# Optimization experiments

Hardware: AMD Instinct MI355X
Metric: run time of the kernel (lower is better)

## Reference

```python
import jax, jax.numpy as jnp
import numpy as np

N = 8192
IN_F = 256
OUT_F = 128

def setup_inputs() -> dict:
    key = jax.random.key(0)
    k1, k2, k3, k4, k5 = jax.random.split(key, 5)
    adjacency_matrix = jax.random.uniform(k1, (N, N), dtype=jnp.float32)
    node_features = jax.random.normal(k2, (N, IN_F), dtype=jnp.float32)
    # nn.Linear(in_features, out_features): W is [out, in], b is [out]
    W = jax.random.normal(k3, (OUT_F, IN_F), dtype=jnp.float32) / np.sqrt(IN_F)
    b = jax.random.normal(k4, (OUT_F,), dtype=jnp.float32) * 0.01
    attn_weights = jax.random.normal(k5, (OUT_F, OUT_F), dtype=jnp.float32)
    return {"adjacency_matrix": adjacency_matrix, "node_features": node_features,
            "W": W, "b": b, "attn_weights": attn_weights}

def reference(adjacency_matrix, node_features, W, b, attn_weights):
    # h = Linear(node_features): [N, out]
    h = node_features @ W.T + b
    # bilinear scores: h @ (A @ h^T) -> [N, N]
    scores = jnp.einsum('nd,de,me->nm', h, attn_weights, h)
    attn = jax.nn.softmax(scores, axis=1)
    # weighted aggregation: [N, N] @ [N, out]
    h_agg = attn @ h
    return h_agg
```

## Files before the change

kernel.cpp:

```cpp
#include <hip/hip_runtime.h>
#include <hip/hip_bf16.h>
#include <stdint.h>


#define NN 8192
#define INF_ 256
#define D 128
#define BQ 128
#define BK 64
#define KSPLIT 8
#define KSEG (NN / KSPLIT)
#define NTILE (KSEG / BK)
#define L2E 1.44269504088896340736f

typedef __attribute__((ext_vector_type(8))) short bf16x8;
typedef __attribute__((ext_vector_type(8))) unsigned short u16x8;
typedef __attribute__((ext_vector_type(4))) float f32x4;

__device__ __forceinline__ void gld16(const __hip_bfloat16* g, __hip_bfloat16* l) {
    __builtin_amdgcn_global_load_lds(
        (const __attribute__((address_space(1))) unsigned int*)(unsigned long long)(uintptr_t)g,
        (__attribute__((address_space(3))) unsigned int*)(unsigned long long)(uintptr_t)l,
        16, 0, 0);
}

__device__ __forceinline__ size_t k_img(int grow, int c) {
    const int row = grow & 63;
    return (size_t)(grow >> 6) * 8192 + row * 128 + (((c >> 3) ^ (row & 15)) * 8) + (c & 7);
}

__device__ __forceinline__ size_t v_img(int j, int c) {
    const int jj = j & 63;
    const int jt = (jj >> 4) & 3, q = (jj >> 2) & 3, r = jj & 3;
    const int jp = (jt >> 1) * 32 + q * 8 + (jt & 1) * 4 + r;
    return (size_t)(j >> 6) * 8192 + c * 64 + (((jp >> 3) ^ (c & 7)) * 8) + (jp & 7);
}

__global__ __launch_bounds__(256) void prep_kernel(
    const float* __restrict__ X, const float* __restrict__ W,
    const float* __restrict__ bias, const float* __restrict__ A,
    __hip_bfloat16* __restrict__ h_hi, __hip_bfloat16* __restrict__ h_lo,
    __hip_bfloat16* __restrict__ q_hi, __hip_bfloat16* __restrict__ q_lo,
    __hip_bfloat16* __restrict__ htp)
{
    __shared__ float xs[32][INF_];
    __shared__ float hs[32][D];
    const int tid  = threadIdx.x;
    const int row0 = blockIdx.x * 32;

    {
        const f32x4* Xv = (const f32x4*)(X + (size_t)row0 * INF_);
        f32x4* xsv = (f32x4*)&xs[0][0];
        #pragma unroll
        for (int i = 0; i < 8; ++i) xsv[tid + i*256] = Xv[tid + i*256];
    }
    __syncthreads();

    const int c  = tid & 127;
    const int rh = tid >> 7;

    float acc[16];
    #pragma unroll
    for (int r = 0; r < 16; ++r) acc[r] = 0.f;
    const f32x4* Wv = (const f32x4*)(W + (size_t)c * INF_);
    for (int k4 = 0; k4 < INF_/4; ++k4) {
        f32x4 w4 = Wv[k4];
        #pragma unroll
        for (int r = 0; r < 16; ++r) {
            f32x4 x4 = ((const f32x4*)&xs[rh*16 + r][0])[k4];
            acc[r] += x4[0]*w4[0] + x4[1]*w4[1] + x4[2]*w4[2] + x4[3]*w4[3];
        }
    }
    const float bc = bias[c];
    #pragma unroll
    for (int r = 0; r < 16; ++r) {
        const int row = rh*16 + r;
        const int grow = row0 + row;
        const float hv = acc[r] + bc;
        hs[row][c] = hv;
        const __hip_bfloat16 hi = __float2bfloat16(hv);
        const float lo = hv - __bfloat162float(hi);
        h_hi[k_img(grow, c)] = hi;
        h_lo[k_img(grow, c)] = __float2bfloat16(lo);
        htp [v_img(grow, c)] = hi;
    }
    __syncthreads();

    float acc2[16];
    #pragma unroll
    for (int r = 0; r < 16; ++r) acc2[r] = 0.f;
    for (int d4 = 0; d4 < D/4; ++d4) {
        f32x4 hv4[16];
        #pragma unroll
        for (int r = 0; r < 16; ++r) hv4[r] = ((const f32x4*)&hs[rh*16 + r][0])[d4];
        #pragma unroll
        for (int dd = 0; dd < 4; ++dd) {
            const float a = A[(size_t)(d4*4 + dd)*D + c];
            #pragma unroll
            for (int r = 0; r < 16; ++r) acc2[r] += hv4[r][dd] * a;
        }
    }
    #pragma unroll
    for (int r = 0; r < 16; ++r) {
        const int row = rh*16 + r;
        const float tv = acc2[r];
        const __hip_bfloat16 hi = __float2bfloat16(tv);
        const float lo = tv - __bfloat162float(hi);
        q_hi[(size_t)(row0+row)*D + c] = hi;
        q_lo[(size_t)(row0+row)*D + c] = __float2bfloat16(lo);
    }
}

__global__ __launch_bounds__(256, 2) void flash_kernel(
    const __hip_bfloat16* __restrict__ q_hi, const __hip_bfloat16* __restrict__ q_lo,
    const __hip_bfloat16* __restrict__ k_hi, const __hip_bfloat16* __restrict__ k_lo,
    const __hip_bfloat16* __restrict__ htp,
    __hip_bfloat16* __restrict__ opart, float* __restrict__ mpart,
    float* __restrict__ lpart)
{
    __shared__ __hip_bfloat16 khi[BK*128];
    __shared__ __hip_bfloat16 klo[BK*128];
    __shared__ __hip_bfloat16 vt [D*64];

    const int tid  = threadIdx.x;
    const int wave = tid >> 6;
    const int lane = tid & 63;
    const int l16  = lane & 15;
    const int quad = lane >> 4;
    const int bid   = blockIdx.x;
    const int split = bid & 7;
    const int q0    = (bid >> 3) * BQ;
    const int tbase = split * NTILE;

    bf16x8 bqh[2][4], bql[2][4];
    #pragma unroll
    for (int it = 0; it < 2; ++it) {
        const size_t qrow = (size_t)q0 + wave*32 + it*16 + l16;
        const __hip_bfloat16* qhp = q_hi + qrow*D;
        const __hip_bfloat16* qlp = q_lo + qrow*D;
        #pragma unroll
        for (int t = 0; t < 4; ++t) {
            bqh[it][t] = *(const bf16x8*)(qhp + t*32 + quad*8);
            bql[it][t] = *(const bf16x8*)(qlp + t*32 + quad*8);
        }
    }

    f32x4 oacc[2][8];
    #pragma unroll
    for (int it = 0; it < 2; ++it)
        #pragma unroll
        for (int i = 0; i < 8; ++i) oacc[it][i] = (f32x4){0.f, 0.f, 0.f, 0.f};
    float mi[2] = {-1e30f, -1e30f}, li[2] = {0.f, 0.f};

    for (int tile = 0; tile < NTILE; ++tile) {
        const size_t tb = (size_t)(tbase + tile) * 8192;
        __syncthreads();
        #pragma unroll
        for (int i = 0; i < 4; ++i) {
            const int cb = (i*4 + wave) * 64;
            const size_t ge = tb + (size_t)(cb + lane) * 8;
            gld16(k_hi + ge, &khi[cb*8]);
            gld16(k_lo + ge, &klo[cb*8]);
            gld16(htp  + ge, &vt [cb*8]);
        }
        __syncthreads();

        f32x4 st[2][4];
        #pragma unroll
        for (int jt = 0; jt < 4; ++jt) {
            #pragma unroll
            for (int t = 0; t < 4; ++t) {
                const int ko = (jt*16 + l16)*128 + (((t*4 + quad) ^ l16) * 8);
                const bf16x8 ah = *(const bf16x8*)(&khi[ko]);
                const bf16x8 al = *(const bf16x8*)(&klo[ko]);
                #pragma unroll
                for (int it = 0; it < 2; ++it) {
                    f32x4 acc = (t == 0) ? (f32x4){0.f,0.f,0.f,0.f} : st[it][jt];
                    acc = __builtin_amdgcn_mfma_f32_16x16x32_bf16(ah, bql[it][t], acc, 0, 0, 0);
                    acc = __builtin_amdgcn_mfma_f32_16x16x32_bf16(al, bqh[it][t], acc, 0, 0, 0);
                    acc = __builtin_amdgcn_mfma_f32_16x16x32_bf16(ah, bqh[it][t], acc, 0, 0, 0);
                    st[it][jt] = acc;
                }
            }
        }

        bf16x8 pb[2][2];
        #pragma unroll
        for (int it = 0; it < 2; ++it) {
            float vmax = st[it][0][0];
            #pragma unroll
            for (int jt = 0; jt < 4; ++jt)
                #pragma unroll
                for (int r = 0; r < 4; ++r) vmax = fmaxf(vmax, st[it][jt][r]);
            vmax = fmaxf(vmax, __shfl_xor(vmax, 16, 64));
            vmax = fmaxf(vmax, __shfl_xor(vmax, 32, 64));
            const float mnew  = fmaxf(mi[it], vmax);
            const float alpha = exp2f((mi[it] - mnew) * L2E);
            mi[it] = mnew;
            float sum = 0.f;
            #pragma unroll
            for (int jt = 0; jt < 4; ++jt)
                #pragma unroll
                for (int r = 0; r < 4; ++r) {
                    const float pv = exp2f((st[it][jt][r] - mnew) * L2E);
                    st[it][jt][r] = pv;
                    sum += pv;
                }
            sum += __shfl_xor(sum, 16, 64);
            sum += __shfl_xor(sum, 32, 64);
            li[it] = li[it] * alpha + sum;

            #pragma unroll
            for (int r = 0; r < 4; ++r) {
                const float ar = __shfl(alpha, quad*4 + r, 64);
                #pragma unroll
                for (int dt = 0; dt < 8; ++dt) oacc[it][dt][r] *= ar;
            }
            #pragma unroll
            for (int jp = 0; jp < 2; ++jp) {
                bf16x8 f;
                #pragma unroll
                for (int r = 0; r < 4; ++r) {
                    f[r]     = __bfloat16_as_short(__float2bfloat16(st[it][2*jp  ][r]));
                    f[r + 4] = __bfloat16_as_short(__float2bfloat16(st[it][2*jp+1][r]));
                }
                pb[it][jp] = f;
            }
        }

        #pragma unroll
        for (int dt = 0; dt < 8; ++dt) {
            const int vo = (dt*16 + l16)*64;
            #pragma unroll
            for (int jp = 0; jp < 2; ++jp) {
                const bf16x8 bv = *(const bf16x8*)(&vt[vo + (((jp*4 + quad) ^ (l16 & 7)) * 8)]);
                #pragma unroll
                for (int it = 0; it < 2; ++it)
                    oacc[it][dt] = __builtin_amdgcn_mfma_f32_16x16x32_bf16(
                        pb[it][jp], bv, oacc[it][dt], 0, 0, 0);
            }
        }
    }

    __hip_bfloat16* op = opart + ((size_t)split * NN + q0 + wave*32) * D;
    #pragma unroll
    for (int it = 0; it < 2; ++it) {
        const float linv = 1.f / li[it];
        #pragma unroll
        for (int r = 0; r < 4; ++r) {
            const int m = it*16 + quad*4 + r;
            const float lr = __shfl(linv, quad*4 + r, 64);
            #pragma unroll
            for (int dt = 0; dt < 8; ++dt)
                op[(size_t)m*D + dt*16 + l16] = __float2bfloat16(oacc[it][dt][r] * lr);
        }
        if (quad == 0) {
            mpart[(size_t)split*NN + q0 + wave*32 + it*16 + l16] = mi[it];
            lpart[(size_t)split*NN + q0 + wave*32 + it*16 + l16] = li[it];
        }
    }
}

__global__ __launch_bounds__(256) void combine_kernel(
    const __hip_bfloat16* __restrict__ opart, const float* __restrict__ mpart,
    const float* __restrict__ lpart, float* __restrict__ out)
{
    const int idx = blockIdx.x * 256 + threadIdx.x;
    const int q  = idx >> 4;
    const int d8 = (idx & 15) * 8;
    float m = -1e30f;
    #pragma unroll
    for (int s = 0; s < KSPLIT; ++s) m = fmaxf(m, mpart[(size_t)s*NN + q]);
    float z = 0.f, o[8];
    #pragma unroll
    for (int e = 0; e < 8; ++e) o[e] = 0.f;
    #pragma unroll
    for (int s = 0; s < KSPLIT; ++s) {
        const float g = lpart[(size_t)s*NN + q] * exp2f((mpart[(size_t)s*NN + q] - m) * L2E);
        z += g;
        const u16x8 v = *(const u16x8*)(opart + ((size_t)s*NN + q)*D + d8);
        #pragma unroll
        for (int e = 0; e < 8; ++e)
            o[e] += g * __uint_as_float((unsigned)v[e] << 16);
    }
    const float zinv = 1.f / z;
    f32x4 lo, hi;
    #pragma unroll
    for (int e = 0; e < 4; ++e) { lo[e] = o[e] * zinv; hi[e] = o[e+4] * zinv; }
    *(f32x4*)(out + (size_t)q*D + d8)     = lo;
    *(f32x4*)(out + (size_t)q*D + d8 + 4) = hi;
}

extern "C" void kernel_launch(void* const* d_in, const int* in_sizes, int n_in,
                              void* d_out, int out_size, void* d_ws, size_t ws_size,
                              hipStream_t stream)
{
    const float* X = (const float*)d_in[1];
    const float* W = (const float*)d_in[2];
    const float* b = (const float*)d_in[3];
    const float* A = (const float*)d_in[4];
    float* out = (float*)d_out;

    char* ws = (char*)d_ws;
    __hip_bfloat16* h_hi = (__hip_bfloat16*)(ws);
    __hip_bfloat16* h_lo = (__hip_bfloat16*)(ws + (size_t)(2u  << 20));
    __hip_bfloat16* q_hi = (__hip_bfloat16*)(ws + (size_t)(4u  << 20));
    __hip_bfloat16* q_lo = (__hip_bfloat16*)(ws + (size_t)(6u  << 20));
    __hip_bfloat16* htp  = (__hip_bfloat16*)(ws + (size_t)(8u  << 20));
    __hip_bfloat16* opart = (__hip_bfloat16*)(ws + (size_t)(10u << 20));
    float* mpart = (float*)(ws + (size_t)(26u << 20));
    float* lpart = (float*)(ws + (size_t)(26u << 20) + (256u << 10));

    prep_kernel<<<NN/32, 256, 0, stream>>>(X, W, b, A, h_hi, h_lo, q_hi, q_lo, htp);
    flash_kernel<<<(NN/BQ) * KSPLIT, 256, 0, stream>>>(
        q_hi, q_lo, h_hi, h_lo, htp, opart, mpart, lpart);
    combine_kernel<<<(NN*16)/256, 256, 0, stream>>>(opart, mpart, lpart, out);
}
```

Baseline: 422.9 us.

## Prefetch next K/V tile during softmax, add lazy rescale and wave priority

Double-buffers the V tile in LDS and issues the async global-to-LDS loads for the next tile right after the QK MFMAs finish, so the loads overlap softmax and PV work instead of stalling at the start of each iteration. It also skips the online-softmax max update and accumulator rescale unless the new row max exceeds the running max by a threshold. MFMA sections are wrapped in s_setprio so waves in those sections get higher issue priority. The risks are the extra LDS for the V buffer, which may reduce occupancy, and exp values up to e^8 before rescaling, which are still bounded in fp32.

```diff
diff --git a/kernel.cpp b/kernel.cpp
--- a/kernel.cpp
+++ b/kernel.cpp
@@ -12,6 +12,7 @@
 #define KSEG (NN / KSPLIT)
 #define NTILE (KSEG / BK)
 #define L2E 1.44269504088896340736f
+#define RESCALE_THR 8.0f
 
 typedef __attribute__((ext_vector_type(8))) short bf16x8;
 typedef __attribute__((ext_vector_type(8))) unsigned short u16x8;
@@ -120,7 +121,7 @@
 {
     __shared__ __hip_bfloat16 khi[BK*128];
     __shared__ __hip_bfloat16 klo[BK*128];
-    __shared__ __hip_bfloat16 vt [D*64];
+    __shared__ __hip_bfloat16 vt [2*D*64];
 
     const int tid  = threadIdx.x;
     const int wave = tid >> 6;
@@ -145,16 +146,8 @@
         }
     }
 
-    f32x4 oacc[2][8];
-    #pragma unroll
-    for (int it = 0; it < 2; ++it)
-        #pragma unroll
-        for (int i = 0; i < 8; ++i) oacc[it][i] = (f32x4){0.f, 0.f, 0.f, 0.f};
-    float mi[2] = {-1e30f, -1e30f}, li[2] = {0.f, 0.f};
-
-    for (int tile = 0; tile < NTILE; ++tile) {
-        const size_t tb = (size_t)(tbase + tile) * 8192;
-        __syncthreads();
+    {
+        const size_t tb = (size_t)tbase * 8192;
         #pragma unroll
         for (int i = 0; i < 4; ++i) {
             const int cb = (i*4 + wave) * 64;
@@ -163,9 +156,20 @@
             gld16(k_lo + ge, &klo[cb*8]);
             gld16(htp  + ge, &vt [cb*8]);
         }
+    }
+
+    f32x4 oacc[2][8];
+    #pragma unroll
+    for (int it = 0; it < 2; ++it)
+        #pragma unroll
+        for (int i = 0; i < 8; ++i) oacc[it][i] = (f32x4){0.f, 0.f, 0.f, 0.f};
+    float mi[2] = {-1e30f, -1e30f}, li[2] = {0.f, 0.f};
+
+    for (int tile = 0; tile < NTILE; ++tile) {
         __syncthreads();
 
         f32x4 st[2][4];
+        __builtin_amdgcn_s_setprio(1);
         #pragma unroll
         for (int jt = 0; jt < 4; ++jt) {
             #pragma unroll
@@ -183,6 +187,23 @@
                 }
             }
         }
+        __builtin_amdgcn_s_setprio(0);
+
+        __syncthreads();
+
+        if (tile + 1 < NTILE) {
+            const size_t tb = (size_t)(tbase + tile + 1) * 8192;
+            const int vb = ((tile + 1) & 1) * (D*64);
+            #pragma unroll
+            for (int i = 0; i < 4; ++i) {
+                const int cb = (i*4 + wave) * 64;
+                const size_t ge = tb + (size_t)(cb + lane) * 8;
+                gld16(k_hi + ge, &khi[cb*8]);
+                gld16(k_lo + ge, &klo[cb*8]);
+                gld16(htp  + ge, &vt [vb + cb*8]);
+            }
+        }
+        __builtin_amdgcn_sched_barrier(0);
 
         bf16x8 pb[2][2];
         #pragma unroll
@@ -194,28 +215,31 @@
                 for (int r = 0; r < 4; ++r) vmax = fmaxf(vmax, st[it][jt][r]);
             vmax = fmaxf(vmax, __shfl_xor(vmax, 16, 64));
             vmax = fmaxf(vmax, __shfl_xor(vmax, 32, 64));
-            const float mnew  = fmaxf(mi[it], vmax);
-            const float alpha = exp2f((mi[it] - mnew) * L2E);
-            mi[it] = mnew;
+            if (!__all(vmax <= mi[it] + RESCALE_THR)) {
+                const float mnew  = fmaxf(mi[it], vmax);
+                const float alpha = exp2f((mi[it] - mnew) * L2E);
+                mi[it] = mnew;
+                li[it] *= alpha;
+                #pragma unroll
+                for (int r = 0; r < 4; ++r) {
+                    const float ar = __shfl(alpha, quad*4 + r, 64);
+                    #pragma unroll
+                    for (int dt = 0; dt < 8; ++dt) oacc[it][dt][r] *= ar;
+                }
+            }
+            const float mcur = mi[it];
             float sum = 0.f;
             #pragma unroll
             for (int jt = 0; jt < 4; ++jt)
                 #pragma unroll
                 for (int r = 0; r < 4; ++r) {
-                    const float pv = exp2f((st[it][jt][r] - mnew) * L2E);
+                    const float pv = exp2f((st[it][jt][r] - mcur) * L2E);
                     st[it][jt][r] = pv;
                     sum += pv;
                 }
             sum += __shfl_xor(sum, 16, 64);
             sum += __shfl_xor(sum, 32, 64);
-            li[it] = li[it] * alpha + sum;
-
-            #pragma unroll
-            for (int r = 0; r < 4; ++r) {
-                const float ar = __shfl(alpha, quad*4 + r, 64);
-                #pragma unroll
-                for (int dt = 0; dt < 8; ++dt) oacc[it][dt][r] *= ar;
-            }
+            li[it] += sum;
             #pragma unroll
             for (int jp = 0; jp < 2; ++jp) {
                 bf16x8 f;
@@ -228,9 +252,11 @@
             }
         }
 
+        const int vr = (tile & 1) * (D*64);
+        __builtin_amdgcn_s_setprio(1);
         #pragma unroll
         for (int dt = 0; dt < 8; ++dt) {
-            const int vo = (dt*16 + l16)*64;
+            const int vo = vr + (dt*16 + l16)*64;
             #pragma unroll
             for (int jp = 0; jp < 2; ++jp) {
                 const bf16x8 bv = *(const bf16x8*)(&vt[vo + (((jp*4 + quad) ^ (l16 & 7)) * 8)]);
@@ -240,6 +266,7 @@
                         pb[it][jp], bv, oacc[it][dt], 0, 0, 0);
             }
         }
+        __builtin_amdgcn_s_setprio(0);
     }
 
     __hip_bfloat16* op = opart + ((size_t)split * NN + q0 + wave*32) * D;
```

After: 420.4 us. Within noise of the previous version (-0.6%).
